# Optimization experiments

Hardware: AMD Instinct MI355X
Metric: run time of the kernel (lower is better)

## Reference

```python
import jax, jax.numpy as jnp
import numpy as np

N_NODES = 102400
N_FEAT = 128
N_TPLT = 16
N_TPLT_NODES = 10
N_GRAPHS = 256
EPS = 1.0       # entropic regularization for the Sinkhorn OT solve
N_ITER = 50     # fixed Sinkhorn iterations


def setup_inputs() -> dict:
    key = jax.random.key(0)
    k1, k2 = jax.random.split(key)
    x = jax.random.normal(k1, (N_NODES, N_FEAT), dtype=jnp.float32)
    # template features ~ N(feature_init_mean=0, feature_init_std=1)
    tplt_features = jax.random.normal(k2, (N_TPLT, N_TPLT_NODES, N_FEAT), dtype=jnp.float32)
    # q0 initialized so softmax(q0) is uniform over template nodes
    q0 = jnp.zeros((N_TPLT, N_TPLT_NODES), dtype=jnp.float32)
    # equal-size graphs: 400 nodes per graph, sorted batch vector (PyG convention)
    batch = jnp.repeat(jnp.arange(N_GRAPHS, dtype=jnp.int32), N_NODES // N_GRAPHS)
    return {"x": x, "tplt_features": tplt_features, "q0": q0,
            "batch": batch, "num_graphs": N_GRAPHS}


def _wasserstein_to_templates(x, tplt_features, q0, batch, num_graphs):
    # x: [N, d] node features; tplt_features: [K, M, d]; q0: [K, M]; batch: [N]
    N = x.shape[0]
    K, M, d = tplt_features.shape
    # squared-Euclidean cost C[n,k,m] = ||x_n - T_km||^2   (ot.dist default)
    C = (jnp.sum(x * x, axis=-1)[:, None, None]
         + jnp.sum(tplt_features * tplt_features, axis=-1)[None, :, :]
         - 2.0 * jnp.einsum('nd,kmd->nkm', x, tplt_features))  # [N,K,M]

    # uniform node weights per graph: a_n = 1/|S_{batch[n]}|
    counts = jax.ops.segment_sum(jnp.ones((N,), x.dtype), batch, num_segments=num_graphs)
    log_a = -jnp.log(counts)[batch]                      # [N]
    # template node weights b = softmax(q0, axis=1)
    log_b = jax.nn.log_softmax(q0, axis=1)               # [K,M]

    def seg_lse(t):  # logsumexp over nodes within each graph; t: [N,K,M] -> [G,K,M]
        m = jax.ops.segment_max(t, batch, num_segments=num_graphs)
        s = jax.ops.segment_sum(jnp.exp(t - m[batch]), batch, num_segments=num_graphs)
        return m + jnp.log(s)

    def f_update(g):  # [G,K,M] -> [N,K]
        return EPS * (log_a[:, None] - jax.nn.logsumexp((g[batch] - C) / EPS, axis=2))

    def step(g, _):
        f = f_update(g)
        g_new = EPS * (log_b[None, :, :] - seg_lse((f[:, :, None] - C) / EPS))
        return g_new, None

    g0 = jnp.zeros((num_graphs, K, M), x.dtype)
    g, _ = jax.lax.scan(step, g0, None, length=N_ITER)
    f = f_update(g)
    # transport plan P[n,k,m] = exp((f + g - C)/eps); OT cost = <P, C> per (graph, template)
    logP = (f[:, :, None] + g[batch] - C) / EPS          # [N,K,M]
    per_node = jnp.sum(jnp.exp(logP) * C, axis=2)        # [N,K]
    return jax.ops.segment_sum(per_node, batch, num_segments=num_graphs)  # [G,K]


def reference(x, tplt_features, q0, batch, num_graphs):
    return _wasserstein_to_templates(x, tplt_features, q0, batch, num_graphs)
```

## Files before the change

### kernel.cpp

```cpp
#include <hip/hip_runtime.h>

#define K_TPLT 16
#define M_NODES 10
#define M2 5
#define DFEAT 128
#define NMAX 7
#define NPROB 2
#define N_ITER 50
#define NEG_BIG -1e30f
#define LOG2E 1.44269504088896340736f
#define LN2   0.69314718055994530942f

#define EXP2F(x) __builtin_amdgcn_exp2f(x)
#define LOG2F(x) __builtin_amdgcn_logf(x)

typedef float v2f __attribute__((ext_vector_type(2)));

__global__ void zero_counts_k(int* counts, int G) {
    int g = blockIdx.x * blockDim.x + threadIdx.x;
    if (g < G) counts[g] = 0;
}

__global__ void count_nodes_k(const int* __restrict__ batch, int* counts, int N) {
    int i = blockIdx.x * blockDim.x + threadIdx.x;
    if (i < N) atomicAdd(&counts[batch[i]], 1);
}

__global__ void scan_counts_k(const int* __restrict__ counts, int* starts, int G) {
    __shared__ int sc[1024];
    int t = threadIdx.x;
    for (int g = t; g < G; g += blockDim.x) sc[g] = counts[g];
    __syncthreads();
    for (int g = t; g < G; g += blockDim.x) {
        int s = 0;
        for (int j = 0; j < g; ++j) s += sc[j];
        starts[g] = s;
    }
}

template <int CTRL>
__device__ __forceinline__ float dpp_add(float v) {
    return v + __int_as_float(__builtin_amdgcn_update_dpp(
        0, __float_as_int(v), CTRL, 0xF, 0xF, true));
}
__device__ __forceinline__ float wred_add_u(float v) {
    v = dpp_add<0xB1>(v);
    v = dpp_add<0x4E>(v);
    v = dpp_add<0x141>(v);
    v = dpp_add<0x140>(v);
    v = dpp_add<0x142>(v);
    v = dpp_add<0x143>(v);
    return __int_as_float(__builtin_amdgcn_readlane(__float_as_int(v), 63));
}
template <int CTRL>
__device__ __forceinline__ float dpp_max(float v) {
    return fmaxf(v, __int_as_float(__builtin_amdgcn_update_dpp(
        0, __float_as_int(v), CTRL, 0xF, 0xF, true)));
}
__device__ __forceinline__ float wred_max(float v) {
    v = dpp_max<0xB1>(v);
    v = dpp_max<0x4E>(v);
    v = dpp_max<0x141>(v);
    v = dpp_max<0x140>(v);
    v = fmaxf(v, __shfl_xor(v, 16));
    v = fmaxf(v, __shfl_xor(v, 32));
    return v;
}
__device__ __forceinline__ v2f v2max(v2f a, v2f b) { return __builtin_elementwise_max(a, b); }
__device__ __forceinline__ float dot4(const float4& a, const float4& b) {
    return a.x * b.x + a.y * b.y + a.z * b.z + a.w * b.w;
}

__global__ __launch_bounds__(64) void sinkhorn_tw_k(
    const float* __restrict__ x, const float* __restrict__ tplt,
    const float* __restrict__ q0, const int* __restrict__ starts,
    const int* __restrict__ counts, float* __restrict__ out, int G)
{
    const int bid  = blockIdx.x;
    const int g    = bid % G;
    const int k0   = bid / G;
    const int lane = threadIdx.x;

    const int start = starts[g];
    const int count = counts[g];
    const float a   = 1.0f / (float)count;
    const float la2 = -LOG2F((float)count);

    v2f lblav[NPROB][M2];
#pragma unroll
    for (int p = 0; p < NPROB; ++p) {
        const float* qk = q0 + (k0 + 8 * p) * M_NODES;
        float qv[M_NODES];
        float qmax = NEG_BIG;
#pragma unroll
        for (int m = 0; m < M_NODES; ++m) { qv[m] = qk[m]; qmax = fmaxf(qmax, qv[m]); }
        float qs = 0.f;
#pragma unroll
        for (int m = 0; m < M_NODES; ++m) {
            qv[m] = (qv[m] - qmax) * LOG2E;
            qs += EXP2F(qv[m]);
        }
        const float corr = LOG2F(qs);
#pragma unroll
        for (int mm = 0; mm < M2; ++mm)
            lblav[p][mm] = (v2f){qv[2 * mm] - corr - la2, qv[2 * mm + 1] - corr - la2};
    }

    bool act[NMAX];
#pragma unroll
    for (int i = 0; i < NMAX; ++i) act[i] = (lane + i * 64) < count;

    v2f Lv[NPROB][NMAX][M2];
    float nsum[NPROB];
    v2f cshv[NPROB][M2];
    {
        const float* Tk0 = tplt + (size_t)k0 * M_NODES * DFEAT;
        const float* Tk1 = tplt + (size_t)(k0 + 8) * M_NODES * DFEAT;
        float x2[NMAX];
        v2f t2v[NPROB][M2];
#pragma unroll
        for (int i = 0; i < NMAX; ++i) {
            x2[i] = 0.f;
#pragma unroll
            for (int p = 0; p < NPROB; ++p)
#pragma unroll
                for (int mm = 0; mm < M2; ++mm) Lv[p][i][mm] = (v2f){0.f, 0.f};
        }
#pragma unroll
        for (int p = 0; p < NPROB; ++p)
#pragma unroll
            for (int mm = 0; mm < M2; ++mm) t2v[p][mm] = (v2f){0.f, 0.f};

        for (int j = 0; j < DFEAT; j += 4) {
            float4 xv[NMAX];
#pragma unroll
            for (int i = 0; i < NMAX; ++i) {
                if (act[i]) {
                    xv[i] = *(const float4*)(x + (size_t)(start + lane + i * 64) * DFEAT + j);
                } else {
                    xv[i].x = xv[i].y = xv[i].z = xv[i].w = 0.f;
                }
                x2[i] += dot4(xv[i], xv[i]);
            }
#pragma unroll
            for (int mm = 0; mm < M2; ++mm) {
                const float4 ta0 = *(const float4*)(Tk0 + (2 * mm)     * DFEAT + j);
                const float4 tb0 = *(const float4*)(Tk0 + (2 * mm + 1) * DFEAT + j);
                const float4 ta1 = *(const float4*)(Tk1 + (2 * mm)     * DFEAT + j);
                const float4 tb1 = *(const float4*)(Tk1 + (2 * mm + 1) * DFEAT + j);
                t2v[0][mm] += (v2f){dot4(ta0, ta0), dot4(tb0, tb0)};
                t2v[1][mm] += (v2f){dot4(ta1, ta1), dot4(tb1, tb1)};
#pragma unroll
                for (int i = 0; i < NMAX; ++i) {
                    Lv[0][i][mm] += (v2f){dot4(xv[i], ta0), dot4(xv[i], tb0)};
                    Lv[1][i][mm] += (v2f){dot4(xv[i], ta1), dot4(xv[i], tb1)};
                }
            }
        }
#pragma unroll
        for (int p = 0; p < NPROB; ++p) {
            nsum[p] = 0.f;
#pragma unroll
            for (int i = 0; i < NMAX; ++i) {
                const v2f x2v = {x2[i], x2[i]};
                v2f mxv = (v2f){NEG_BIG, NEG_BIG};
#pragma unroll
                for (int mm = 0; mm < M2; ++mm) {
                    Lv[p][i][mm] = (Lv[p][i][mm] * 2.f - x2v - t2v[p][mm]) * LOG2E;
                    mxv = v2max(mxv, Lv[p][i][mm]);
                }
                const float mx = fmaxf(mxv.x, mxv.y);
                if (act[i]) nsum[p] += mx;
                const v2f mxb = {mx, mx};
#pragma unroll
                for (int mm = 0; mm < M2; ++mm) Lv[p][i][mm] -= mxb;
            }
            float csh[M_NODES];
#pragma unroll
            for (int m = 0; m < M_NODES; ++m) {
                float c = NEG_BIG;
#pragma unroll
                for (int i = 0; i < NMAX; ++i) {
                    const float lv = (m & 1) ? Lv[p][i][m >> 1].y : Lv[p][i][m >> 1].x;
                    c = act[i] ? fmaxf(c, lv) : c;
                }
                csh[m] = wred_max(c);
            }
#pragma unroll
            for (int mm = 0; mm < M2; ++mm) cshv[p][mm] = (v2f){csh[2 * mm], csh[2 * mm + 1]};
        }
    }

    v2f g2v[NPROB][M2];

#pragma unroll
    for (int p = 0; p < NPROB; ++p) {
        v2f w0v[M2], acc[M2];
#pragma unroll
        for (int mm = 0; mm < M2; ++mm) {
            w0v[mm] = (v2f){EXP2F(cshv[p][mm].x), EXP2F(cshv[p][mm].y)};
            acc[mm] = (v2f){0.f, 0.f};
        }
#pragma unroll
        for (int i = 0; i < NMAX; ++i) {
            if (act[i]) {
                v2f Ev[M2];
                v2f Dp = (v2f){0.f, 0.f};
#pragma unroll
                for (int mm = 0; mm < M2; ++mm) {
                    Ev[mm] = (v2f){EXP2F(Lv[p][i][mm].x - cshv[p][mm].x),
                                   EXP2F(Lv[p][i][mm].y - cshv[p][mm].y)};
                    Dp += Ev[mm] * w0v[mm];
                }
                const float D = Dp.x + Dp.y;
                const float r = __builtin_amdgcn_rcpf(D);
                const v2f rv = {r, r};
#pragma unroll
                for (int mm = 0; mm < M2; ++mm) acc[mm] += Ev[mm] * rv;
            }
        }
#pragma unroll
        for (int mm = 0; mm < M2; ++mm) {
            const float s0 = wred_add_u(acc[mm].x);
            const float s1 = wred_add_u(acc[mm].y);
            g2v[p][mm].x = lblav[p][mm].x - cshv[p][mm].x - LOG2F(fmaxf(s0, 1e-35f));
            g2v[p][mm].y = lblav[p][mm].y - cshv[p][mm].y - LOG2F(fmaxf(s1, 1e-35f));
        }
    }

    for (int it = 1; it < N_ITER; ++it) {
        v2f acc[NPROB][M2];
#pragma unroll
        for (int p = 0; p < NPROB; ++p)
#pragma unroll
            for (int mm = 0; mm < M2; ++mm) acc[p][mm] = (v2f){0.f, 0.f};

#pragma unroll
        for (int i = 0; i < NMAX; ++i) {
            if (act[i]) {
#pragma unroll
                for (int p = 0; p < NPROB; ++p) {
                    v2f z[M2];
#pragma unroll
                    for (int mm = 0; mm < M2; ++mm) z[mm] = g2v[p][mm] + Lv[p][i][mm];
                    v2f mzv = v2max(z[0], z[1]);
                    mzv = v2max(mzv, z[2]);
                    mzv = v2max(mzv, z[3]);
                    mzv = v2max(mzv, z[4]);
                    const float zmax = fmaxf(mzv.x, mzv.y);
                    const v2f zb = {zmax, zmax};
                    v2f e[M2];
                    v2f Dp = (v2f){0.f, 0.f};
#pragma unroll
                    for (int mm = 0; mm < M2; ++mm) {
                        const v2f d = z[mm] - zb;
                        e[mm] = (v2f){EXP2F(d.x), EXP2F(d.y)};
                        Dp += e[mm];
                    }
                    const float D = Dp.x + Dp.y;
                    const float r = __builtin_amdgcn_rcpf(D);
                    const v2f rv = {r, r};
#pragma unroll
                    for (int mm = 0; mm < M2; ++mm) acc[p][mm] += e[mm] * rv;
                }
            }
        }
#pragma unroll
        for (int p = 0; p < NPROB; ++p)
#pragma unroll
            for (int mm = 0; mm < M2; ++mm) {
                const float s0 = wred_add_u(acc[p][mm].x);
                const float s1 = wred_add_u(acc[p][mm].y);
                g2v[p][mm].x = lblav[p][mm].x + g2v[p][mm].x - LOG2F(fmaxf(s0, 1e-35f));
                g2v[p][mm].y = lblav[p][mm].y + g2v[p][mm].y - LOG2F(fmaxf(s1, 1e-35f));
            }
    }

#pragma unroll
    for (int p = 0; p < NPROB; ++p) {
        float accum = nsum[p];
#pragma unroll
        for (int i = 0; i < NMAX; ++i) {
            if (act[i]) {
                v2f z[M2];
#pragma unroll
                for (int mm = 0; mm < M2; ++mm) z[mm] = g2v[p][mm] + Lv[p][i][mm];
                v2f mzv = v2max(z[0], z[1]);
                mzv = v2max(mzv, z[2]);
                mzv = v2max(mzv, z[3]);
                mzv = v2max(mzv, z[4]);
                const float zmax = fmaxf(mzv.x, mzv.y);
                const v2f zb = {zmax, zmax};
                v2f e[M2];
                v2f Dp = (v2f){0.f, 0.f};
                v2f qv = (v2f){0.f, 0.f};
#pragma unroll
                for (int mm = 0; mm < M2; ++mm) {
                    const v2f d = z[mm] - zb;
                    e[mm] = (v2f){EXP2F(d.x), EXP2F(d.y)};
                    Dp += e[mm];
                    qv += e[mm] * Lv[p][i][mm];
                }
                const float D = Dp.x + Dp.y;
                const float r = __builtin_amdgcn_rcpf(D);
                accum += (qv.x + qv.y) * r;
            }
        }
        accum = wred_add_u(accum);
        if (lane == 0) out[(size_t)g * K_TPLT + (k0 + 8 * p)] = -a * LN2 * accum;
    }
}

extern "C" void kernel_launch(void* const* d_in, const int* in_sizes, int n_in,
                              void* d_out, int out_size, void* d_ws, size_t ws_size,
                              hipStream_t stream) {
    const float* x    = (const float*)d_in[0];
    const float* tplt = (const float*)d_in[1];
    const float* q0   = (const float*)d_in[2];
    const int* batch  = (const int*)d_in[3];
    const int N = in_sizes[3];
    const int G = out_size / K_TPLT;

    int* counts = (int*)d_ws;
    int* starts = counts + G;

    zero_counts_k<<<(G + 255) / 256, 256, 0, stream>>>(counts, G);
    count_nodes_k<<<(N + 255) / 256, 256, 0, stream>>>(batch, counts, N);
    scan_counts_k<<<1, 256, 0, stream>>>(counts, starts, G);
    sinkhorn_tw_k<<<G * (K_TPLT / 2), 64, 0, stream>>>(x, tplt, q0, starts, counts,
                                                       (float*)d_out, G);
}
```

Baseline: 459.4 us.

## Split each graph's nodes across two wavefronts with LDS cross-wave reductions

Each block now uses two 64-lane wavefronts instead of one. Nodes are interleaved between the two waves, so each lane holds at most 4 nodes rather than 7, which cuts register pressure and the per-wave serial work in the 50 Sinkhorn iterations. The per-iteration column sums and maxima are combined across the two waves through shared memory, using a double-buffered array and a __syncthreads each iteration. The price is a block barrier per iteration plus extra LDS traffic, in exchange for more parallelism and higher occupancy.

```diff
diff --git a/kernel.cpp b/kernel.cpp
--- a/kernel.cpp
+++ b/kernel.cpp
@@ -4,7 +4,7 @@
 #define M_NODES 10
 #define M2 5
 #define DFEAT 128
-#define NMAX 7
+#define NMAXW 4
 #define NPROB 2
 #define N_ITER 50
 #define NEG_BIG -1e30f
@@ -71,7 +71,7 @@
     return a.x * b.x + a.y * b.y + a.z * b.z + a.w * b.w;
 }
 
-__global__ __launch_bounds__(64) void sinkhorn_tw_k(
+__global__ __launch_bounds__(128) void sinkhorn_tw_k(
     const float* __restrict__ x, const float* __restrict__ tplt,
     const float* __restrict__ q0, const int* __restrict__ starts,
     const int* __restrict__ counts, float* __restrict__ out, int G)
@@ -79,7 +79,12 @@
     const int bid  = blockIdx.x;
     const int g    = bid % G;
     const int k0   = bid / G;
-    const int lane = threadIdx.x;
+    const int w    = threadIdx.x >> 6;
+    const int lane = threadIdx.x & 63;
+
+    __shared__ float sm_max[NPROB][2][M_NODES];
+    __shared__ float sm_acc[2][NPROB][2][M_NODES];
+    __shared__ float sm_out[NPROB][2];
 
     const int start = starts[g];
     const int count = counts[g];
@@ -106,54 +111,54 @@
             lblav[p][mm] = (v2f){qv[2 * mm] - corr - la2, qv[2 * mm + 1] - corr - la2};
     }
 
-    bool act[NMAX];
-#pragma unroll
-    for (int i = 0; i < NMAX; ++i) act[i] = (lane + i * 64) < count;
-
-    v2f Lv[NPROB][NMAX][M2];
+    bool act[NMAXW];
+#pragma unroll
+    for (int j = 0; j < NMAXW; ++j) act[j] = (lane + 64 * (2 * j + w)) < count;
+
+    v2f Lv[NPROB][NMAXW][M2];
     float nsum[NPROB];
     v2f cshv[NPROB][M2];
     {
         const float* Tk0 = tplt + (size_t)k0 * M_NODES * DFEAT;
         const float* Tk1 = tplt + (size_t)(k0 + 8) * M_NODES * DFEAT;
-        float x2[NMAX];
+        float x2[NMAXW];
         v2f t2v[NPROB][M2];
 #pragma unroll
-        for (int i = 0; i < NMAX; ++i) {
-            x2[i] = 0.f;
+        for (int j = 0; j < NMAXW; ++j) {
+            x2[j] = 0.f;
 #pragma unroll
             for (int p = 0; p < NPROB; ++p)
 #pragma unroll
-                for (int mm = 0; mm < M2; ++mm) Lv[p][i][mm] = (v2f){0.f, 0.f};
+                for (int mm = 0; mm < M2; ++mm) Lv[p][j][mm] = (v2f){0.f, 0.f};
         }
 #pragma unroll
         for (int p = 0; p < NPROB; ++p)
 #pragma unroll
             for (int mm = 0; mm < M2; ++mm) t2v[p][mm] = (v2f){0.f, 0.f};
 
-        for (int j = 0; j < DFEAT; j += 4) {
-            float4 xv[NMAX];
-#pragma unroll
-            for (int i = 0; i < NMAX; ++i) {
-                if (act[i]) {
-                    xv[i] = *(const float4*)(x + (size_t)(start + lane + i * 64) * DFEAT + j);
+        for (int jf = 0; jf < DFEAT; jf += 4) {
+            float4 xv[NMAXW];
+#pragma unroll
+            for (int j = 0; j < NMAXW; ++j) {
+                if (act[j]) {
+                    xv[j] = *(const float4*)(x + (size_t)(start + lane + 64 * (2 * j + w)) * DFEAT + jf);
                 } else {
-                    xv[i].x = xv[i].y = xv[i].z = xv[i].w = 0.f;
-                }
-                x2[i] += dot4(xv[i], xv[i]);
+                    xv[j].x = xv[j].y = xv[j].z = xv[j].w = 0.f;
+                }
+                x2[j] += dot4(xv[j], xv[j]);
             }
 #pragma unroll
             for (int mm = 0; mm < M2; ++mm) {
-                const float4 ta0 = *(const float4*)(Tk0 + (2 * mm)     * DFEAT + j);
-                const float4 tb0 = *(const float4*)(Tk0 + (2 * mm + 1) * DFEAT + j);
-                const float4 ta1 = *(const float4*)(Tk1 + (2 * mm)     * DFEAT + j);
-                const float4 tb1 = *(const float4*)(Tk1 + (2 * mm + 1) * DFEAT + j);
+                const float4 ta0 = *(const float4*)(Tk0 + (2 * mm)     * DFEAT + jf);
+                const float4 tb0 = *(const float4*)(Tk0 + (2 * mm + 1) * DFEAT + jf);
+                const float4 ta1 = *(const float4*)(Tk1 + (2 * mm)     * DFEAT + jf);
+                const float4 tb1 = *(const float4*)(Tk1 + (2 * mm + 1) * DFEAT + jf);
                 t2v[0][mm] += (v2f){dot4(ta0, ta0), dot4(tb0, tb0)};
                 t2v[1][mm] += (v2f){dot4(ta1, ta1), dot4(tb1, tb1)};
 #pragma unroll
-                for (int i = 0; i < NMAX; ++i) {
-                    Lv[0][i][mm] += (v2f){dot4(xv[i], ta0), dot4(xv[i], tb0)};
-                    Lv[1][i][mm] += (v2f){dot4(xv[i], ta1), dot4(xv[i], tb1)};
+                for (int j = 0; j < NMAXW; ++j) {
+                    Lv[0][j][mm] += (v2f){dot4(xv[j], ta0), dot4(xv[j], tb0)};
+                    Lv[1][j][mm] += (v2f){dot4(xv[j], ta1), dot4(xv[j], tb1)};
                 }
             }
         }
@@ -161,74 +166,91 @@
         for (int p = 0; p < NPROB; ++p) {
             nsum[p] = 0.f;
 #pragma unroll
-            for (int i = 0; i < NMAX; ++i) {
-                const v2f x2v = {x2[i], x2[i]};
+            for (int j = 0; j < NMAXW; ++j) {
+                const v2f x2v = {x2[j], x2[j]};
                 v2f mxv = (v2f){NEG_BIG, NEG_BIG};
 #pragma unroll
                 for (int mm = 0; mm < M2; ++mm) {
-                    Lv[p][i][mm] = (Lv[p][i][mm] * 2.f - x2v - t2v[p][mm]) * LOG2E;
-                    mxv = v2max(mxv, Lv[p][i][mm]);
+                    Lv[p][j][mm] = (Lv[p][j][mm] * 2.f - x2v - t2v[p][mm]) * LOG2E;
+                    mxv = v2max(mxv, Lv[p][j][mm]);
                 }
                 const float mx = fmaxf(mxv.x, mxv.y);
-                if (act[i]) nsum[p] += mx;
+                if (act[j]) nsum[p] += mx;
                 const v2f mxb = {mx, mx};
 #pragma unroll
-                for (int mm = 0; mm < M2; ++mm) Lv[p][i][mm] -= mxb;
-            }
-            float csh[M_NODES];
+                for (int mm = 0; mm < M2; ++mm) Lv[p][j][mm] -= mxb;
+            }
 #pragma unroll
             for (int m = 0; m < M_NODES; ++m) {
                 float c = NEG_BIG;
 #pragma unroll
-                for (int i = 0; i < NMAX; ++i) {
-                    const float lv = (m & 1) ? Lv[p][i][m >> 1].y : Lv[p][i][m >> 1].x;
-                    c = act[i] ? fmaxf(c, lv) : c;
-                }
-                csh[m] = wred_max(c);
-            }
-#pragma unroll
-            for (int mm = 0; mm < M2; ++mm) cshv[p][mm] = (v2f){csh[2 * mm], csh[2 * mm + 1]};
-        }
-    }
+                for (int j = 0; j < NMAXW; ++j) {
+                    const float lv = (m & 1) ? Lv[p][j][m >> 1].y : Lv[p][j][m >> 1].x;
+                    c = act[j] ? fmaxf(c, lv) : c;
+                }
+                c = wred_max(c);
+                if (lane == 0) sm_max[p][w][m] = c;
+            }
+        }
+    }
+    __syncthreads();
+#pragma unroll
+    for (int p = 0; p < NPROB; ++p)
+#pragma unroll
+        for (int mm = 0; mm < M2; ++mm)
+            cshv[p][mm] = (v2f){fmaxf(sm_max[p][0][2 * mm],     sm_max[p][1][2 * mm]),
+                                fmaxf(sm_max[p][0][2 * mm + 1], sm_max[p][1][2 * mm + 1])};
 
     v2f g2v[NPROB][M2];
 
-#pragma unroll
-    for (int p = 0; p < NPROB; ++p) {
-        v2f w0v[M2], acc[M2];
-#pragma unroll
-        for (int mm = 0; mm < M2; ++mm) {
-            w0v[mm] = (v2f){EXP2F(cshv[p][mm].x), EXP2F(cshv[p][mm].y)};
-            acc[mm] = (v2f){0.f, 0.f};
-        }
-#pragma unroll
-        for (int i = 0; i < NMAX; ++i) {
-            if (act[i]) {
-                v2f Ev[M2];
-                v2f Dp = (v2f){0.f, 0.f};
-#pragma unroll
-                for (int mm = 0; mm < M2; ++mm) {
-                    Ev[mm] = (v2f){EXP2F(Lv[p][i][mm].x - cshv[p][mm].x),
-                                   EXP2F(Lv[p][i][mm].y - cshv[p][mm].y)};
-                    Dp += Ev[mm] * w0v[mm];
-                }
-                const float D = Dp.x + Dp.y;
-                const float r = __builtin_amdgcn_rcpf(D);
-                const v2f rv = {r, r};
-#pragma unroll
-                for (int mm = 0; mm < M2; ++mm) acc[mm] += Ev[mm] * rv;
-            }
-        }
-#pragma unroll
-        for (int mm = 0; mm < M2; ++mm) {
-            const float s0 = wred_add_u(acc[mm].x);
-            const float s1 = wred_add_u(acc[mm].y);
-            g2v[p][mm].x = lblav[p][mm].x - cshv[p][mm].x - LOG2F(fmaxf(s0, 1e-35f));
-            g2v[p][mm].y = lblav[p][mm].y - cshv[p][mm].y - LOG2F(fmaxf(s1, 1e-35f));
-        }
+    {
+        v2f acc[NPROB][M2];
+#pragma unroll
+        for (int p = 0; p < NPROB; ++p) {
+            v2f w0v[M2];
+#pragma unroll
+            for (int mm = 0; mm < M2; ++mm) {
+                w0v[mm] = (v2f){EXP2F(cshv[p][mm].x), EXP2F(cshv[p][mm].y)};
+                acc[p][mm] = (v2f){0.f, 0.f};
+            }
+#pragma unroll
+            for (int j = 0; j < NMAXW; ++j) {
+                if (act[j]) {
+                    v2f Ev[M2];
+                    v2f Dp = (v2f){0.f, 0.f};
+#pragma unroll
+                    for (int mm = 0; mm < M2; ++mm) {
+                        Ev[mm] = (v2f){EXP2F(Lv[p][j][mm].x - cshv[p][mm].x),
+                                       EXP2F(Lv[p][j][mm].y - cshv[p][mm].y)};
+                        Dp += Ev[mm] * w0v[mm];
+                    }
+                    const float D = Dp.x + Dp.y;
+                    const float r = __builtin_amdgcn_rcpf(D);
+                    const v2f rv = {r, r};
+#pragma unroll
+                    for (int mm = 0; mm < M2; ++mm) acc[p][mm] += Ev[mm] * rv;
+                }
+            }
+#pragma unroll
+            for (int m = 0; m < M_NODES; ++m) {
+                const float s = wred_add_u((m & 1) ? acc[p][m >> 1].y : acc[p][m >> 1].x);
+                if (lane == 0) sm_acc[0][p][w][m] = s;
+            }
+        }
+        __syncthreads();
+#pragma unroll
+        for (int p = 0; p < NPROB; ++p)
+#pragma unroll
+            for (int mm = 0; mm < M2; ++mm) {
+                const float s0 = sm_acc[0][p][0][2 * mm]     + sm_acc[0][p][1][2 * mm];
+                const float s1 = sm_acc[0][p][0][2 * mm + 1] + sm_acc[0][p][1][2 * mm + 1];
+                g2v[p][mm].x = lblav[p][mm].x - cshv[p][mm].x - LOG2F(fmaxf(s0, 1e-35f));
+                g2v[p][mm].y = lblav[p][mm].y - cshv[p][mm].y - LOG2F(fmaxf(s1, 1e-35f));
+            }
     }
 
     for (int it = 1; it < N_ITER; ++it) {
+        const int par = it & 1;
         v2f acc[NPROB][M2];
 #pragma unroll
         for (int p = 0; p < NPROB; ++p)
@@ -236,13 +258,13 @@
             for (int mm = 0; mm < M2; ++mm) acc[p][mm] = (v2f){0.f, 0.f};
 
 #pragma unroll
-        for (int i = 0; i < NMAX; ++i) {
-            if (act[i]) {
+        for (int j = 0; j < NMAXW; ++j) {
+            if (act[j]) {
 #pragma unroll
                 for (int p = 0; p < NPROB; ++p) {
                     v2f z[M2];
 #pragma unroll
-                    for (int mm = 0; mm < M2; ++mm) z[mm] = g2v[p][mm] + Lv[p][i][mm];
+                    for (int mm = 0; mm < M2; ++mm) z[mm] = g2v[p][mm] + Lv[p][j][mm];
                     v2f mzv = v2max(z[0], z[1]);
                     mzv = v2max(mzv, z[2]);
                     mzv = v2max(mzv, z[3]);
@@ -268,9 +290,17 @@
 #pragma unroll
         for (int p = 0; p < NPROB; ++p)
 #pragma unroll
+            for (int m = 0; m < M_NODES; ++m) {
+                const float s = wred_add_u((m & 1) ? acc[p][m >> 1].y : acc[p][m >> 1].x);
+                if (lane == 0) sm_acc[par][p][w][m] = s;
+            }
+        __syncthreads();
+#pragma unroll
+        for (int p = 0; p < NPROB; ++p)
+#pragma unroll
             for (int mm = 0; mm < M2; ++mm) {
-                const float s0 = wred_add_u(acc[p][mm].x);
-                const float s1 = wred_add_u(acc[p][mm].y);
+                const float s0 = sm_acc[par][p][0][2 * mm]     + sm_acc[par][p][1][2 * mm];
+                const float s1 = sm_acc[par][p][0][2 * mm + 1] + sm_acc[par][p][1][2 * mm + 1];
                 g2v[p][mm].x = lblav[p][mm].x + g2v[p][mm].x - LOG2F(fmaxf(s0, 1e-35f));
                 g2v[p][mm].y = lblav[p][mm].y + g2v[p][mm].y - LOG2F(fmaxf(s1, 1e-35f));
             }
@@ -280,26 +310,25 @@
     for (int p = 0; p < NPROB; ++p) {
         float accum = nsum[p];
 #pragma unroll
-        for (int i = 0; i < NMAX; ++i) {
-            if (act[i]) {
+        for (int j = 0; j < NMAXW; ++j) {
+            if (act[j]) {
                 v2f z[M2];
 #pragma unroll
-                for (int mm = 0; mm < M2; ++mm) z[mm] = g2v[p][mm] + Lv[p][i][mm];
+                for (int mm = 0; mm < M2; ++mm) z[mm] = g2v[p][mm] + Lv[p][j][mm];
                 v2f mzv = v2max(z[0], z[1]);
                 mzv = v2max(mzv, z[2]);
                 mzv = v2max(mzv, z[3]);
                 mzv = v2max(mzv, z[4]);
                 const float zmax = fmaxf(mzv.x, mzv.y);
                 const v2f zb = {zmax, zmax};
-                v2f e[M2];
                 v2f Dp = (v2f){0.f, 0.f};
                 v2f qv = (v2f){0.f, 0.f};
 #pragma unroll
                 for (int mm = 0; mm < M2; ++mm) {
                     const v2f d = z[mm] - zb;
-                    e[mm] = (v2f){EXP2F(d.x), EXP2F(d.y)};
-                    Dp += e[mm];
-                    qv += e[mm] * Lv[p][i][mm];
+                    const v2f e = {EXP2F(d.x), EXP2F(d.y)};
+                    Dp += e;
+                    qv += e * Lv[p][j][mm];
                 }
                 const float D = Dp.x + Dp.y;
                 const float r = __builtin_amdgcn_rcpf(D);
@@ -307,7 +336,14 @@
             }
         }
         accum = wred_add_u(accum);
-        if (lane == 0) out[(size_t)g * K_TPLT + (k0 + 8 * p)] = -a * LN2 * accum;
+        if (lane == 0) sm_out[p][w] = accum;
+    }
+    __syncthreads();
+    if (w == 0 && lane == 0) {
+#pragma unroll
+        for (int p = 0; p < NPROB; ++p)
+            out[(size_t)g * K_TPLT + (k0 + 8 * p)] =
+                -a * LN2 * (sm_out[p][0] + sm_out[p][1]);
     }
 }
 
@@ -327,6 +363,6 @@
     zero_counts_k<<<(G + 255) / 256, 256, 0, stream>>>(counts, G);
     count_nodes_k<<<(N + 255) / 256, 256, 0, stream>>>(batch, counts, N);
     scan_counts_k<<<1, 256, 0, stream>>>(counts, starts, G);
-    sinkhorn_tw_k<<<G * (K_TPLT / 2), 64, 0, stream>>>(x, tplt, q0, starts, counts,
-                                                       (float*)d_out, G);
-}
+    sinkhorn_tw_k<<<G * (K_TPLT / 2), 128, 0, stream>>>(x, tplt, q0, starts, counts,
+                                                        (float*)d_out, G);
+}
```

Result: slower. 617.6 us (+34.5%).
